# Optimization experiments

Hardware: AMD Instinct MI355X
Metric: run time of the kernel (lower is better)

Reference implementation:

```python
import jax, jax.numpy as jnp
import numpy as np

ALPHA = 0.2  # LeakyReLU negative slope
NEG_INF = jnp.float32(-9e15)


def setup_inputs() -> dict:
    key = jax.random.key(0)
    k1, k2, k3, k4, k5, k6 = jax.random.split(key, 6)
    B, N, F_in, F_out = 8, 2048, 256, 64
    h = jax.random.normal(k1, (B, N, F_in), dtype=jnp.float32)
    adj = jax.random.randint(k2, (B, N, N), 0, 2, dtype=jnp.int32)
    level = jax.random.uniform(k3, (B, N), dtype=jnp.float32)
    node_type = jax.random.uniform(k4, (B, N, N), dtype=jnp.float32)
    W = jax.random.normal(k5, (F_in, F_out), dtype=jnp.float32) * 1.414 / np.sqrt(F_in)
    a = jax.random.normal(k6, (2 * F_out, 1), dtype=jnp.float32) * 1.414 / np.sqrt(2 * F_out)
    return {"h": h, "adj": adj, "level": level, "node_type": node_type, "W": W, "a": a}


def reference(h, adj, level, node_type, W, a):
    # h: [B,N,Fin], adj/node_type: [B,N,N], level: [B,N], W: [Fin,Fout], a: [2*Fout,1]
    F_out = W.shape[1]
    Wh = jnp.einsum('bnf,fo->bno', h, W)  # [B,N,Fout]
    # Additive attention decomposed: e[b,i,j] = a1.Wh_i + a2.Wh_j (no O(N^2*2F) tensor)
    a1 = a[:F_out, 0]
    a2 = a[F_out:, 0]
    f1 = Wh @ a1  # [B,N]
    f2 = Wh @ a2  # [B,N]
    e = jax.nn.leaky_relu(f1[:, :, None] + f2[:, None, :], negative_slope=ALPHA)  # [B,N,N]
    # gat_our=True path: node_type scales scores, level scales Wh
    e = e * node_type
    Wh = Wh * level[:, :, None]
    attention = jnp.where(adj > 0, e, NEG_INF)
    attention = jax.nn.softmax(attention, axis=1)  # faithful: original softmax over dim=1
    # dropout p=0 / eval mode -> identity
    h_prime = jnp.einsum('bij,bjo->bio', attention, Wh)  # [B,N,Fout]
    return jax.nn.relu(h_prime)  # concat=True
```

## Files before the change

### kernel.cpp

```cpp
#include <hip/hip_runtime.h>

#define BB 8
#define NN 2048
#define FIN 256
#define FO 64

typedef short short8_t __attribute__((ext_vector_type(8)));
typedef float float4_t __attribute__((ext_vector_type(4)));
typedef int int4_v __attribute__((ext_vector_type(4)));

__device__ __forceinline__ unsigned short f2bf(float x) {
  unsigned int u = __float_as_uint(x);
  unsigned int r = (u + 0x7fffu + ((u >> 16) & 1u)) >> 16;
  return (unsigned short)r;
}

#define GLD16(gp, lp)                                                          \
  __builtin_amdgcn_global_load_lds(                                            \
      (const __attribute__((address_space(1))) void*)(gp),                     \
      (__attribute__((address_space(3))) void*)(lp), 16, 0, 0)

__global__ __launch_bounds__(256) void k1_fused(
    const float* __restrict__ h,
    const float* __restrict__ level,
    const float* __restrict__ W,
    const float* __restrict__ a,
    float* __restrict__ V, float* __restrict__ f1, float* __restrict__ f2,
    float* __restrict__ scol,
    const int* __restrict__ adj,
    unsigned int* __restrict__ abits)
{
  __shared__ float wlds[128 * 64];
  __shared__ float hs[16 * 260];
  __shared__ float parts1[16 * 17];
  __shared__ float parts2[16 * 17];
  int t = threadIdx.x;

  if (blockIdx.x >= 1024) {
    size_t g = (size_t)(blockIdx.x - 1024) * 256 + t;
    const int4_v* ap = (const int4_v*)adj + g * 8;
    int4_v av[8];
    #pragma unroll
    for (int e = 0; e < 8; ++e) av[e] = ap[e];
    unsigned int m = 0;
    #pragma unroll
    for (int e = 0; e < 8; ++e) {
      m |= (av[e].x > 0 ? 1u : 0u) << (4 * e);
      m |= (av[e].y > 0 ? 1u : 0u) << (4 * e + 1);
      m |= (av[e].z > 0 ? 1u : 0u) << (4 * e + 2);
      m |= (av[e].w > 0 ? 1u : 0u) << (4 * e + 3);
    }
    abits[g] = m;
    return;
  }

  int b = blockIdx.x >> 7;
  int i0 = (blockIdx.x & 127) * 16;

  if (blockIdx.x < 64) scol[blockIdx.x * 256 + t] = 0.0f;

  {
    int r_ld = t >> 4, f0 = (t & 15) * 16;
    const float* hp = h + (size_t)(b * NN + i0 + r_ld) * FIN + f0;
    float4 x0 = *(const float4*)(hp);
    float4 x1 = *(const float4*)(hp + 4);
    float4 x2 = *(const float4*)(hp + 8);
    float4 x3 = *(const float4*)(hp + 12);
    float* hd = &hs[r_ld * 260 + f0];
    *(float4*)(hd + 0) = x0; *(float4*)(hd + 4) = x1;
    *(float4*)(hd + 8) = x2; *(float4*)(hd + 12) = x3;
  }

  int r = t >> 4;
  int c4 = (t & 15) * 4;
  float4 acc = {0, 0, 0, 0};

  #pragma unroll
  for (int half = 0; half < 2; ++half) {
    __syncthreads();
    #pragma unroll
    for (int q = 0; q < 8; ++q) {
      int idx = q * 1024 + t * 4;
      *(float4*)&wlds[idx] = *(const float4*)&W[half * 8192 + idx];
    }
    __syncthreads();
    for (int f = 0; f < 128; f += 8) {
      float4 hv0 = *(const float4*)&hs[r * 260 + half * 128 + f];
      float4 hv1 = *(const float4*)&hs[r * 260 + half * 128 + f + 4];
      float hvv[8] = {hv0.x, hv0.y, hv0.z, hv0.w, hv1.x, hv1.y, hv1.z, hv1.w};
      #pragma unroll
      for (int k = 0; k < 8; ++k) {
        float4 wv = *(const float4*)&wlds[(f + k) * 64 + c4];
        acc.x += hvv[k] * wv.x; acc.y += hvv[k] * wv.y;
        acc.z += hvv[k] * wv.z; acc.w += hvv[k] * wv.w;
      }
    }
  }

  float p1 = acc.x * a[c4] + acc.y * a[c4 + 1] + acc.z * a[c4 + 2] + acc.w * a[c4 + 3];
  float p2 = acc.x * a[64 + c4] + acc.y * a[64 + c4 + 1] +
             acc.z * a[64 + c4 + 2] + acc.w * a[64 + c4 + 3];
  parts1[r * 17 + (t & 15)] = p1;
  parts2[r * 17 + (t & 15)] = p2;
  __syncthreads();
  if (t < 16) {
    float s1 = 0.f, s2 = 0.f;
    #pragma unroll
    for (int g = 0; g < 16; ++g) { s1 += parts1[t * 17 + g]; s2 += parts2[t * 17 + g]; }
    f1[b * NN + i0 + t] = s1;
    f2[b * NN + i0 + t] = s2;
  }

  float lv = level[b * NN + i0 + r];
  float4 vv = {acc.x * lv, acc.y * lv, acc.z * lv, acc.w * lv};
  *(float4*)&V[(size_t)(b * NN + i0 + r) * FO + c4] = vv;
}

__global__ __launch_bounds__(512) void k2a_stream(
    const unsigned int* __restrict__ abits,
    const float* __restrict__ ntp,
    const float* __restrict__ f1,
    const float* __restrict__ f2,
    unsigned short* __restrict__ u_bf,
    float* __restrict__ partials)
{
  __shared__ unsigned int lbits[32 * 64];
  __shared__ float sf1[32];
  int t = threadIdx.x;
  int b = blockIdx.x >> 6;
  int rowblk = blockIdx.x & 63;
  int row0 = rowblk * 32;
  size_t base = (size_t)b * NN;
  int j0 = t * 4;

  {
    const uint4* src = (const uint4*)(abits + (base + row0) * 64);
    ((uint4*)lbits)[t] = src[t];
    if (t < 32) sf1[t] = f1[base + row0 + t];
  }

  float4 f2v = *(const float4*)(f2 + base + j0);
  float acc0 = 0.f, acc1 = 0.f, acc2 = 0.f, acc3 = 0.f;

  size_t rb = (base + row0) * (size_t)NN + j0;
  const float* np = ntp + rb;
  unsigned short* up = u_bf + rb;
  int wrd = t >> 3;
  int sh = (t & 7) * 4;

  __syncthreads();

  #pragma unroll
  for (int g = 0; g < 4; ++g) {
    float4 nv[8];
    #pragma unroll
    for (int rr = 0; rr < 8; ++rr)
      nv[rr] = *(const float4*)(np + (size_t)(g * 8 + rr) * NN);
    #pragma unroll
    for (int rr = 0; rr < 8; ++rr) {
      int r = g * 8 + rr;
      unsigned int nib = lbits[r * 64 + wrd] >> sh;
      float f1v = sf1[r];
      float x0 = f1v + f2v.x; x0 = fmaxf(x0, 0.2f * x0);
      float x1 = f1v + f2v.y; x1 = fmaxf(x1, 0.2f * x1);
      float x2 = f1v + f2v.z; x2 = fmaxf(x2, 0.2f * x2);
      float x3 = f1v + f2v.w; x3 = fmaxf(x3, 0.2f * x3);
      float u0 = (nib & 1u) ? __expf(x0 * nv[rr].x) : 0.0f;
      float u1 = (nib & 2u) ? __expf(x1 * nv[rr].y) : 0.0f;
      float u2 = (nib & 4u) ? __expf(x2 * nv[rr].z) : 0.0f;
      float u3 = (nib & 8u) ? __expf(x3 * nv[rr].w) : 0.0f;
      acc0 += u0; acc1 += u1; acc2 += u2; acc3 += u3;
      unsigned int p0 = (unsigned int)f2bf(u0) | ((unsigned int)f2bf(u1) << 16);
      unsigned int p1 = (unsigned int)f2bf(u2) | ((unsigned int)f2bf(u3) << 16);
      *(uint2*)(up + (size_t)r * NN) = make_uint2(p0, p1);
    }
  }

  *(float4*)(partials + (size_t)(b * 64 + rowblk) * NN + j0) =
      make_float4(acc0, acc1, acc2, acc3);
}

__global__ __launch_bounds__(512) void k2a_stream_adj(
    const int* __restrict__ adj,
    const float* __restrict__ ntp,
    const float* __restrict__ f1,
    const float* __restrict__ f2,
    unsigned short* __restrict__ u_bf,
    float* __restrict__ partials)
{
  int t = threadIdx.x;
  int b = blockIdx.x >> 6;
  int rowblk = blockIdx.x & 63;
  int row0 = rowblk * 32;
  size_t base = (size_t)b * NN;
  int j0 = t * 4;

  float4 f2v = *(const float4*)(f2 + base + j0);
  float acc0 = 0.f, acc1 = 0.f, acc2 = 0.f, acc3 = 0.f;

  size_t rb = (base + row0) * (size_t)NN + j0;
  const int* ap = adj + rb;
  const float* np = ntp + rb;
  unsigned short* up = u_bf + rb;
  const float* f1p = f1 + base + row0;

  #pragma unroll
  for (int g = 0; g < 4; ++g) {
    int4 av[8];
    float4 nv[8];
    #pragma unroll
    for (int rr = 0; rr < 8; ++rr) {
      av[rr] = *(const int4*)(ap + (size_t)(g * 8 + rr) * NN);
      nv[rr] = *(const float4*)(np + (size_t)(g * 8 + rr) * NN);
    }
    #pragma unroll
    for (int rr = 0; rr < 8; ++rr) {
      float f1v = f1p[g * 8 + rr];
      float x0 = f1v + f2v.x; x0 = fmaxf(x0, 0.2f * x0);
      float x1 = f1v + f2v.y; x1 = fmaxf(x1, 0.2f * x1);
      float x2 = f1v + f2v.z; x2 = fmaxf(x2, 0.2f * x2);
      float x3 = f1v + f2v.w; x3 = fmaxf(x3, 0.2f * x3);
      float u0 = (av[rr].x > 0) ? __expf(x0 * nv[rr].x) : 0.0f;
      float u1 = (av[rr].y > 0) ? __expf(x1 * nv[rr].y) : 0.0f;
      float u2 = (av[rr].z > 0) ? __expf(x2 * nv[rr].z) : 0.0f;
      float u3 = (av[rr].w > 0) ? __expf(x3 * nv[rr].w) : 0.0f;
      acc0 += u0; acc1 += u1; acc2 += u2; acc3 += u3;
      unsigned int p0 = (unsigned int)f2bf(u0) | ((unsigned int)f2bf(u1) << 16);
      unsigned int p1 = (unsigned int)f2bf(u2) | ((unsigned int)f2bf(u3) << 16);
      *(uint2*)(up + (size_t)(g * 8 + rr) * NN) = make_uint2(p0, p1);
    }
  }

  *(float4*)(partials + (size_t)(b * 64 + rowblk) * NN + j0) =
      make_float4(acc0, acc1, acc2, acc3);
}

template <int STORE_U>
__global__ __launch_bounds__(512) void k2a_stats(
    const int* __restrict__ adj,
    const float* __restrict__ ntp,
    const float* __restrict__ f1,
    const float* __restrict__ f2,
    unsigned short* __restrict__ u_bf,
    unsigned char* __restrict__ bits,
    float* __restrict__ scol)
{
  __shared__ int ladj[2][16 * 256];
  __shared__ float lnt[2][16 * 256];
  __shared__ float red[2048];
  int t = threadIdx.x;
  int b = blockIdx.x >> 6;
  int row0 = (blockIdx.x & 63) * 32;
  int w = t >> 6, l = t & 63;
  size_t base = (size_t)b * NN;

  auto stage = [&](int buf, int s) {
    int tile = s >> 3, c = s & 7;
    int r0 = row0 + tile * 16 + 2 * w;
    const int* ga = adj + (base + r0) * NN + c * 256 + l * 4;
    const float* gn = ntp + (base + r0) * NN + c * 256 + l * 4;
    GLD16(ga, &ladj[buf][(2 * w) * 256]);
    GLD16(ga + NN, &ladj[buf][(2 * w + 1) * 256]);
    GLD16(gn, &lnt[buf][(2 * w) * 256]);
    GLD16(gn + NN, &lnt[buf][(2 * w + 1) * 256]);
  };

  int jj = t & 255;
  int rh = t >> 8;

  float accJ[8];
  #pragma unroll
  for (int c = 0; c < 8; ++c) accJ[c] = 0.f;
  float f2v[8];
  #pragma unroll
  for (int c = 0; c < 8; ++c) f2v[c] = f2[base + c * 256 + jj];

  stage(0, 0);
  for (int s = 0; s < 16; ++s) {
    int buf = s & 1;
    __syncthreads();
    if (s < 15) stage(buf ^ 1, s + 1);
    int tile = s >> 3, c = s & 7;
    #pragma unroll
    for (int q = 0; q < 8; ++q) {
      int r = rh * 8 + q;
      int av = ladj[buf][r * 256 + jj];
      float nv = lnt[buf][r * 256 + jj];
      float f1v = f1[base + row0 + tile * 16 + r];
      float x = f1v + f2v[c];
      x = fmaxf(x, 0.2f * x);
      bool m = av > 0;
      float u = m ? __expf(x * nv) : 0.0f;
      accJ[c] += u;
      if (STORE_U) {
        u_bf[(base + row0 + tile * 16 + r) * NN + c * 256 + jj] = f2bf(u);
      } else {
        unsigned long long bal = __ballot(m);
        if (l == 0)
          *(unsigned long long*)&bits[(base + row0 + tile * 16 + r) * (NN / 8)
                                      + c * 32 + (w & 3) * 8] = bal;
      }
    }
  }

  if (rh == 0) {
    #pragma unroll
    for (int c = 0; c < 8; ++c) red[c * 256 + jj] = accJ[c];
  }
  __syncthreads();
  if (rh == 1) {
    #pragma unroll
    for (int c = 0; c < 8; ++c) red[c * 256 + jj] += accJ[c];
  }
  __syncthreads();
  #pragma unroll
  for (int q = 0; q < 4; ++q)
    atomicAdd(&scol[base + q * 512 + t], red[q * 512 + t]);
}

__global__ __launch_bounds__(256) void k2b_pack_p(
    const float* __restrict__ V,
    const float* __restrict__ partials,
    unsigned short* __restrict__ vf)
{
  __shared__ float sred[8 * 32];
  __shared__ float sinv[32];
  int t = threadIdx.x;
  int b = blockIdx.x >> 6;
  int kk = blockIdx.x & 63;

  {
    int tj = t & 31, tr = t >> 5;
    float s = 0.f;
    #pragma unroll
    for (int q = 0; q < 8; ++q)
      s += partials[(size_t)(b * 64 + tr * 8 + q) * NN + kk * 32 + tj];
    sred[tr * 32 + tj] = s;
  }
  __syncthreads();
  if (t < 32) {
    float tot = 0.f;
    #pragma unroll
    for (int g = 0; g < 8; ++g) tot += sred[g * 32 + t];
    sinv[t] = (tot > 0.f) ? (1.0f / tot) : 0.0f;
  }
  __syncthreads();

  int ng = t >> 6;
  int l = t & 63;
  int jb0 = (l >> 4) * 8;
  int jb = kk * 32 + jb0;
  int o = ng * 16 + (l & 15);
  unsigned int pk[4];
  #pragma unroll
  for (int p = 0; p < 4; ++p) {
    int jr0 = jb + 2 * p, jr1 = jb + 2 * p + 1;
    float i0 = sinv[jb0 + 2 * p];
    float i1 = sinv[jb0 + 2 * p + 1];
    float v0 = V[(size_t)(b * NN + jr0) * FO + o] * i0;
    float v1 = V[(size_t)(b * NN + jr1) * FO + o] * i1;
    pk[p] = (unsigned int)f2bf(v0) | ((unsigned int)f2bf(v1) << 16);
  }
  *(uint4*)(vf + (size_t)(((b * 64 + kk) * 4 + ng) * 64 + l) * 8) =
      make_uint4(pk[0], pk[1], pk[2], pk[3]);
}

__global__ __launch_bounds__(256) void k2b_pack(
    const float* __restrict__ V,
    const float* __restrict__ scol,
    unsigned short* __restrict__ vf)
{
  int t = threadIdx.x;
  int b = blockIdx.x >> 6;
  int kk = blockIdx.x & 63;
  int ng = t >> 6;
  int l = t & 63;
  int jb = kk * 32 + ((l >> 4) * 8);
  int o = ng * 16 + (l & 15);
  unsigned int pk[4];
  #pragma unroll
  for (int p = 0; p < 4; ++p) {
    int jr0 = jb + 2 * p, jr1 = jb + 2 * p + 1;
    float s0 = scol[b * NN + jr0];
    float s1 = scol[b * NN + jr1];
    float i0 = (s0 > 0.f) ? (1.0f / s0) : 0.0f;
    float i1 = (s1 > 0.f) ? (1.0f / s1) : 0.0f;
    float v0 = V[(size_t)(b * NN + jr0) * FO + o] * i0;
    float v1 = V[(size_t)(b * NN + jr1) * FO + o] * i1;
    pk[p] = (unsigned int)f2bf(v0) | ((unsigned int)f2bf(v1) << 16);
  }
  *(uint4*)(vf + (size_t)(((b * 64 + kk) * 4 + ng) * 64 + l) * 8) =
      make_uint4(pk[0], pk[1], pk[2], pk[3]);
}

__global__ __launch_bounds__(512, 4) void k3_agg_u3(
    const unsigned short* __restrict__ u_bf,
    const unsigned short* __restrict__ vf,
    float* __restrict__ outp)
{
  __shared__ float red[8 * 16 * 68];
  int t = threadIdx.x;
  int b = blockIdx.x >> 6;
  int tt = blockIdx.x & 63;
  int i0 = tt * 32;
  int w = t >> 6, l = t & 63;
  int col = l & 15, quad = l >> 4;
  const unsigned short* urow0 = u_bf + (size_t)(b * NN + i0 + col) * NN + quad * 8;
  const unsigned short* urow1 = urow0 + (size_t)16 * NN;
  const unsigned short* vbase = vf + (size_t)(b * 64) * 2048 + l * 8;

  float4_t acc[2][4];
  #pragma unroll
  for (int sgi = 0; sgi < 2; ++sgi)
    #pragma unroll
    for (int g = 0; g < 4; ++g) acc[sgi][g] = (float4_t){0, 0, 0, 0};

  int kk0 = w * 8;
  short8_t A0 = *(const short8_t*)(urow0 + kk0 * 32);
  short8_t A1 = *(const short8_t*)(urow1 + kk0 * 32);
  const unsigned short* vb0 = vbase + (size_t)kk0 * 2048;
  short8_t c0 = *(const short8_t*)(vb0);
  short8_t c1 = *(const short8_t*)(vb0 + 512);
  short8_t c2 = *(const short8_t*)(vb0 + 1024);
  short8_t c3 = *(const short8_t*)(vb0 + 1536);

  #pragma unroll
  for (int s = 0; s < 8; ++s) {
    short8_t nA0, nA1, n0, n1, n2, n3;
    if (s < 7) {
      int kk = w * 8 + s + 1;
      nA0 = *(const short8_t*)(urow0 + kk * 32);
      nA1 = *(const short8_t*)(urow1 + kk * 32);
      const unsigned short* vn = vbase + (size_t)kk * 2048;
      n0 = *(const short8_t*)(vn);
      n1 = *(const short8_t*)(vn + 512);
      n2 = *(const short8_t*)(vn + 1024);
      n3 = *(const short8_t*)(vn + 1536);
    }
    acc[0][0] = __builtin_amdgcn_mfma_f32_16x16x32_bf16(A0, c0, acc[0][0], 0, 0, 0);
    acc[0][1] = __builtin_amdgcn_mfma_f32_16x16x32_bf16(A0, c1, acc[0][1], 0, 0, 0);
    acc[0][2] = __builtin_amdgcn_mfma_f32_16x16x32_bf16(A0, c2, acc[0][2], 0, 0, 0);
    acc[0][3] = __builtin_amdgcn_mfma_f32_16x16x32_bf16(A0, c3, acc[0][3], 0, 0, 0);
    acc[1][0] = __builtin_amdgcn_mfma_f32_16x16x32_bf16(A1, c0, acc[1][0], 0, 0, 0);
    acc[1][1] = __builtin_amdgcn_mfma_f32_16x16x32_bf16(A1, c1, acc[1][1], 0, 0, 0);
    acc[1][2] = __builtin_amdgcn_mfma_f32_16x16x32_bf16(A1, c2, acc[1][2], 0, 0, 0);
    acc[1][3] = __builtin_amdgcn_mfma_f32_16x16x32_bf16(A1, c3, acc[1][3], 0, 0, 0);
    if (s < 7) { A0 = nA0; A1 = nA1; c0 = n0; c1 = n1; c2 = n2; c3 = n3; }
  }

  #pragma unroll
  for (int sub = 0; sub < 2; ++sub) {
    __syncthreads();
    #pragma unroll
    for (int r = 0; r < 4; ++r) {
      int rowi = quad * 4 + r;
      float* rp = &red[w * 1088 + rowi * 68 + col];
      rp[0] = acc[sub][0][r];
      rp[16] = acc[sub][1][r];
      rp[32] = acc[sub][2][r];
      rp[48] = acc[sub][3][r];
    }
    __syncthreads();
    if (t < 256) {
      int row = t >> 4, o4 = (t & 15) * 4;
      const float* rp = &red[row * 68 + o4];
      float4 s0 = *(const float4*)(rp);
      float4 s1 = *(const float4*)(rp + 1088);
      float4 s2 = *(const float4*)(rp + 2176);
      float4 s3 = *(const float4*)(rp + 3264);
      float4 s4 = *(const float4*)(rp + 4352);
      float4 s5 = *(const float4*)(rp + 5440);
      float4 s6 = *(const float4*)(rp + 6528);
      float4 s7 = *(const float4*)(rp + 7616);
      float4 o;
      o.x = fmaxf(s0.x + s1.x + s2.x + s3.x + s4.x + s5.x + s6.x + s7.x, 0.0f);
      o.y = fmaxf(s0.y + s1.y + s2.y + s3.y + s4.y + s5.y + s6.y + s7.y, 0.0f);
      o.z = fmaxf(s0.z + s1.z + s2.z + s3.z + s4.z + s5.z + s6.z + s7.z, 0.0f);
      o.w = fmaxf(s0.w + s1.w + s2.w + s3.w + s4.w + s5.w + s6.w + s7.w, 0.0f);
      *(float4*)&outp[(size_t)(b * NN + i0 + sub * 16 + row) * FO + o4] = o;
    }
  }
}

__global__ __launch_bounds__(256) void k3_agg_b(
    const float* __restrict__ ntp,
    const unsigned char* __restrict__ bits,
    const float* __restrict__ f1,
    const float* __restrict__ f2,
    const unsigned short* __restrict__ vf,
    float* __restrict__ outp)
{
  __shared__ float red[4 * 16 * 68];
  int t = threadIdx.x;
  int b = blockIdx.x >> 7;
  int i0 = (blockIdx.x & 127) * 16;
  int w = t >> 6, l = t & 63;
  int col = l & 15, quad = l >> 4;
  int gi = b * NN + i0 + col;
  float f1v = f1[gi];
  const float* ntrow = ntp + (size_t)gi * NN;
  const unsigned char* brow = bits + (size_t)gi * (NN / 8);
  float4_t acc0 = {0, 0, 0, 0}, acc1 = {0, 0, 0, 0}, acc2 = {0, 0, 0, 0}, acc3 = {0, 0, 0, 0};

  for (int s = 0; s < 16; ++s) {
    int kk = w * 16 + s;
    int jq = kk * 32 + quad * 8;
    unsigned int m8 = brow[jq >> 3];
    float4 n0 = *(const float4*)(ntrow + jq);
    float4 n1 = *(const float4*)(ntrow + jq + 4);
    float4 g0 = *(const float4*)(f2 + b * NN + jq);
    float4 g1 = *(const float4*)(f2 + b * NN + jq + 4);
    float f2v[8] = {g0.x, g0.y, g0.z, g0.w, g1.x, g1.y, g1.z, g1.w};
    float ntf[8] = {n0.x, n0.y, n0.z, n0.w, n1.x, n1.y, n1.z, n1.w};
    union { unsigned int u[4]; short8_t v; } A;
    #pragma unroll
    for (int p = 0; p < 4; ++p) {
      int e0 = 2 * p, e1 = 2 * p + 1;
      float x0 = f1v + f2v[e0]; x0 = fmaxf(x0, 0.2f * x0);
      float u0 = ((m8 >> e0) & 1u) ? __expf(x0 * ntf[e0]) : 0.0f;
      float x1 = f1v + f2v[e1]; x1 = fmaxf(x1, 0.2f * x1);
      float u1 = ((m8 >> e1) & 1u) ? __expf(x1 * ntf[e1]) : 0.0f;
      A.u[p] = (unsigned int)f2bf(u0) | ((unsigned int)f2bf(u1) << 16);
    }
    const unsigned short* vb = vf + (size_t)(b * 64 + kk) * 2048 + l * 8;
    short8_t bf0 = *(const short8_t*)(vb);
    short8_t bf1 = *(const short8_t*)(vb + 512);
    short8_t bf2 = *(const short8_t*)(vb + 1024);
    short8_t bf3 = *(const short8_t*)(vb + 1536);
    acc0 = __builtin_amdgcn_mfma_f32_16x16x32_bf16(A.v, bf0, acc0, 0, 0, 0);
    acc1 = __builtin_amdgcn_mfma_f32_16x16x32_bf16(A.v, bf1, acc1, 0, 0, 0);
    acc2 = __builtin_amdgcn_mfma_f32_16x16x32_bf16(A.v, bf2, acc2, 0, 0, 0);
    acc3 = __builtin_amdgcn_mfma_f32_16x16x32_bf16(A.v, bf3, acc3, 0, 0, 0);
  }

  #pragma unroll
  for (int r = 0; r < 4; ++r) {
    int rowi = quad * 4 + r;
    red[w * 1088 + rowi * 68 + 0 + col] = acc0[r];
    red[w * 1088 + rowi * 68 + 16 + col] = acc1[r];
    red[w * 1088 + rowi * 68 + 32 + col] = acc2[r];
    red[w * 1088 + rowi * 68 + 48 + col] = acc3[r];
  }
  __syncthreads();

  int row = t >> 4, o4 = (t & 15) * 4;
  const float* rp = &red[row * 68 + o4];
  float4 s0 = *(const float4*)(rp);
  float4 s1 = *(const float4*)(rp + 1088);
  float4 s2 = *(const float4*)(rp + 2176);
  float4 s3 = *(const float4*)(rp + 3264);
  float4 o;
  o.x = fmaxf(s0.x + s1.x + s2.x + s3.x, 0.0f);
  o.y = fmaxf(s0.y + s1.y + s2.y + s3.y, 0.0f);
  o.z = fmaxf(s0.z + s1.z + s2.z + s3.z, 0.0f);
  o.w = fmaxf(s0.w + s1.w + s2.w + s3.w, 0.0f);
  *(float4*)&outp[(size_t)(b * NN + i0 + row) * FO + o4] = o;
}

extern "C" void kernel_launch(void* const* d_in, const int* in_sizes, int n_in,
                              void* d_out, int out_size, void* d_ws, size_t ws_size,
                              hipStream_t stream) {
  const float* h = (const float*)d_in[0];
  const int* adj = (const int*)d_in[1];
  const float* level = (const float*)d_in[2];
  const float* ntm = (const float*)d_in[3];
  const float* W = (const float*)d_in[4];
  const float* a = (const float*)d_in[5];
  float* outp = (float*)d_out;

  float* V = (float*)d_ws;
  float* f1 = V + (size_t)BB * NN * FO;
  float* f2 = f1 + BB * NN;
  float* scol = f2 + BB * NN;
  unsigned short* vf = (unsigned short*)(scol + BB * NN);
  float* partials = (float*)(vf + (size_t)BB * NN * FO);
  unsigned int* abits = (unsigned int*)(partials + (size_t)BB * 64 * NN);
  char* tail = (char*)(abits + (size_t)BB * NN * (NN / 32));
  size_t fixed2 = (size_t)(tail - (char*)d_ws);
  size_t fixed1 = (size_t)((char*)abits - (char*)d_ws);
  size_t ubytes = (size_t)BB * NN * NN * 2;
  bool big2 = (ws_size >= fixed2 + ubytes);
  bool big1 = (ws_size >= fixed1 + ubytes);

  if (big2) {
    unsigned short* u_bf = (unsigned short*)tail;
    k1_fused<<<5120, 256, 0, stream>>>(h, level, W, a, V, f1, f2, scol, adj, abits);
    k2a_stream<<<512, 512, 0, stream>>>(abits, ntm, f1, f2, u_bf, partials);
    k2b_pack_p<<<512, 256, 0, stream>>>(V, partials, vf);
    k3_agg_u3<<<512, 512, 0, stream>>>(u_bf, vf, outp);
  } else if (big1) {
    unsigned short* u_bf = (unsigned short*)abits;
    k1_fused<<<1024, 256, 0, stream>>>(h, level, W, a, V, f1, f2, scol, adj, abits);
    k2a_stream_adj<<<512, 512, 0, stream>>>(adj, ntm, f1, f2, u_bf, partials);
    k2b_pack_p<<<512, 256, 0, stream>>>(V, partials, vf);
    k3_agg_u3<<<512, 512, 0, stream>>>(u_bf, vf, outp);
  } else {
    unsigned char* bits = (unsigned char*)abits;
    k1_fused<<<1024, 256, 0, stream>>>(h, level, W, a, V, f1, f2, scol, adj, abits);
    k2a_stats<0><<<512, 512, 0, stream>>>(adj, ntm, f1, f2, nullptr, bits, scol);
    k2b_pack<<<512, 256, 0, stream>>>(V, scol, vf);
    k3_agg_b<<<1024, 256, 0, stream>>>(ntm, bits, f1, f2, vf, outp);
  }
}
```

Before: 326.9 us.

## Interleave adj-pack and GEMM blocks in k1, halve k3 row tile to 16

In k1, the Wh GEMM blocks are now interleaved with the adjacency bit-packing blocks (every fifth block does the GEMM) rather than all sitting at the front of the grid. The W staging tile also shrinks to 64 rows, cutting shared memory so more blocks can fit per CU. The aggregation kernel now handles 16 rows per block with one A fragment, doubling the grid to 1024 blocks and dropping the second reduction pass. This aims to balance load and raise occupancy, at the cost of re-reading the V fragments twice as often across blocks.

```diff
diff --git a/kernel.cpp b/kernel.cpp
--- a/kernel.cpp
+++ b/kernel.cpp
@@ -30,34 +30,41 @@
     const int* __restrict__ adj,
     unsigned int* __restrict__ abits)
 {
-  __shared__ float wlds[128 * 64];
+  __shared__ float wlds[64 * 64];
   __shared__ float hs[16 * 260];
   __shared__ float parts1[16 * 17];
   __shared__ float parts2[16 * 17];
   int t = threadIdx.x;
 
-  if (blockIdx.x >= 1024) {
-    size_t g = (size_t)(blockIdx.x - 1024) * 256 + t;
-    const int4_v* ap = (const int4_v*)adj + g * 8;
-    int4_v av[8];
-    #pragma unroll
-    for (int e = 0; e < 8; ++e) av[e] = ap[e];
-    unsigned int m = 0;
-    #pragma unroll
-    for (int e = 0; e < 8; ++e) {
-      m |= (av[e].x > 0 ? 1u : 0u) << (4 * e);
-      m |= (av[e].y > 0 ? 1u : 0u) << (4 * e + 1);
-      m |= (av[e].z > 0 ? 1u : 0u) << (4 * e + 2);
-      m |= (av[e].w > 0 ? 1u : 0u) << (4 * e + 3);
-    }
-    abits[g] = m;
-    return;
-  }
-
-  int b = blockIdx.x >> 7;
-  int i0 = (blockIdx.x & 127) * 16;
-
-  if (blockIdx.x < 64) scol[blockIdx.x * 256 + t] = 0.0f;
+  int g;
+  if (gridDim.x > 1024) {
+    if ((blockIdx.x % 5) != 0) {
+      size_t sid = (size_t)(blockIdx.x - blockIdx.x / 5 - 1);
+      size_t gg = sid * 256 + t;
+      const int4_v* ap = (const int4_v*)adj + gg * 8;
+      int4_v av[8];
+      #pragma unroll
+      for (int e = 0; e < 8; ++e) av[e] = ap[e];
+      unsigned int m = 0;
+      #pragma unroll
+      for (int e = 0; e < 8; ++e) {
+        m |= (av[e].x > 0 ? 1u : 0u) << (4 * e);
+        m |= (av[e].y > 0 ? 1u : 0u) << (4 * e + 1);
+        m |= (av[e].z > 0 ? 1u : 0u) << (4 * e + 2);
+        m |= (av[e].w > 0 ? 1u : 0u) << (4 * e + 3);
+      }
+      abits[gg] = m;
+      return;
+    }
+    g = blockIdx.x / 5;
+  } else {
+    g = blockIdx.x;
+  }
+
+  int b = g >> 7;
+  int i0 = (g & 127) * 16;
+
+  if (g < 64) scol[g * 256 + t] = 0.0f;
 
   {
     int r_ld = t >> 4, f0 = (t & 15) * 16;
@@ -76,17 +83,17 @@
   float4 acc = {0, 0, 0, 0};
 
   #pragma unroll
-  for (int half = 0; half < 2; ++half) {
+  for (int qtr = 0; qtr < 4; ++qtr) {
     __syncthreads();
     #pragma unroll
-    for (int q = 0; q < 8; ++q) {
+    for (int q = 0; q < 4; ++q) {
       int idx = q * 1024 + t * 4;
-      *(float4*)&wlds[idx] = *(const float4*)&W[half * 8192 + idx];
+      *(float4*)&wlds[idx] = *(const float4*)&W[qtr * 4096 + idx];
     }
     __syncthreads();
-    for (int f = 0; f < 128; f += 8) {
-      float4 hv0 = *(const float4*)&hs[r * 260 + half * 128 + f];
-      float4 hv1 = *(const float4*)&hs[r * 260 + half * 128 + f + 4];
+    for (int f = 0; f < 64; f += 8) {
+      float4 hv0 = *(const float4*)&hs[r * 260 + qtr * 64 + f];
+      float4 hv1 = *(const float4*)&hs[r * 260 + qtr * 64 + f + 4];
       float hvv[8] = {hv0.x, hv0.y, hv0.z, hv0.w, hv1.x, hv1.y, hv1.z, hv1.w};
       #pragma unroll
       for (int k = 0; k < 8; ++k) {
@@ -106,7 +113,7 @@
   if (t < 16) {
     float s1 = 0.f, s2 = 0.f;
     #pragma unroll
-    for (int g = 0; g < 16; ++g) { s1 += parts1[t * 17 + g]; s2 += parts2[t * 17 + g]; }
+    for (int q = 0; q < 16; ++q) { s1 += parts1[t * 17 + q]; s2 += parts2[t * 17 + q]; }
     f1[b * NN + i0 + t] = s1;
     f2[b * NN + i0 + t] = s2;
   }
@@ -393,31 +400,27 @@
       make_uint4(pk[0], pk[1], pk[2], pk[3]);
 }
 
-__global__ __launch_bounds__(512, 4) void k3_agg_u3(
+__global__ __launch_bounds__(512, 4) void k3_agg_u4(
     const unsigned short* __restrict__ u_bf,
     const unsigned short* __restrict__ vf,
     float* __restrict__ outp)
 {
   __shared__ float red[8 * 16 * 68];
   int t = threadIdx.x;
-  int b = blockIdx.x >> 6;
-  int tt = blockIdx.x & 63;
-  int i0 = tt * 32;
+  int b = blockIdx.x >> 7;
+  int tt = blockIdx.x & 127;
+  int i0 = tt * 16;
   int w = t >> 6, l = t & 63;
   int col = l & 15, quad = l >> 4;
   const unsigned short* urow0 = u_bf + (size_t)(b * NN + i0 + col) * NN + quad * 8;
-  const unsigned short* urow1 = urow0 + (size_t)16 * NN;
   const unsigned short* vbase = vf + (size_t)(b * 64) * 2048 + l * 8;
 
-  float4_t acc[2][4];
-  #pragma unroll
-  for (int sgi = 0; sgi < 2; ++sgi)
-    #pragma unroll
-    for (int g = 0; g < 4; ++g) acc[sgi][g] = (float4_t){0, 0, 0, 0};
+  float4_t acc[4];
+  #pragma unroll
+  for (int g = 0; g < 4; ++g) acc[g] = (float4_t){0, 0, 0, 0};
 
   int kk0 = w * 8;
   short8_t A0 = *(const short8_t*)(urow0 + kk0 * 32);
-  short8_t A1 = *(const short8_t*)(urow1 + kk0 * 32);
   const unsigned short* vb0 = vbase + (size_t)kk0 * 2048;
   short8_t c0 = *(const short8_t*)(vb0);
   short8_t c1 = *(const short8_t*)(vb0 + 512);
@@ -426,59 +429,50 @@
 
   #pragma unroll
   for (int s = 0; s < 8; ++s) {
-    short8_t nA0, nA1, n0, n1, n2, n3;
+    short8_t nA0, n0, n1, n2, n3;
     if (s < 7) {
       int kk = w * 8 + s + 1;
       nA0 = *(const short8_t*)(urow0 + kk * 32);
-      nA1 = *(const short8_t*)(urow1 + kk * 32);
       const unsigned short* vn = vbase + (size_t)kk * 2048;
       n0 = *(const short8_t*)(vn);
       n1 = *(const short8_t*)(vn + 512);
       n2 = *(const short8_t*)(vn + 1024);
       n3 = *(const short8_t*)(vn + 1536);
     }
-    acc[0][0] = __builtin_amdgcn_mfma_f32_16x16x32_bf16(A0, c0, acc[0][0], 0, 0, 0);
-    acc[0][1] = __builtin_amdgcn_mfma_f32_16x16x32_bf16(A0, c1, acc[0][1], 0, 0, 0);
-    acc[0][2] = __builtin_amdgcn_mfma_f32_16x16x32_bf16(A0, c2, acc[0][2], 0, 0, 0);
-    acc[0][3] = __builtin_amdgcn_mfma_f32_16x16x32_bf16(A0, c3, acc[0][3], 0, 0, 0);
-    acc[1][0] = __builtin_amdgcn_mfma_f32_16x16x32_bf16(A1, c0, acc[1][0], 0, 0, 0);
-    acc[1][1] = __builtin_amdgcn_mfma_f32_16x16x32_bf16(A1, c1, acc[1][1], 0, 0, 0);
-    acc[1][2] = __builtin_amdgcn_mfma_f32_16x16x32_bf16(A1, c2, acc[1][2], 0, 0, 0);
-    acc[1][3] = __builtin_amdgcn_mfma_f32_16x16x32_bf16(A1, c3, acc[1][3], 0, 0, 0);
-    if (s < 7) { A0 = nA0; A1 = nA1; c0 = n0; c1 = n1; c2 = n2; c3 = n3; }
-  }
-
-  #pragma unroll
-  for (int sub = 0; sub < 2; ++sub) {
-    __syncthreads();
-    #pragma unroll
-    for (int r = 0; r < 4; ++r) {
-      int rowi = quad * 4 + r;
-      float* rp = &red[w * 1088 + rowi * 68 + col];
-      rp[0] = acc[sub][0][r];
-      rp[16] = acc[sub][1][r];
-      rp[32] = acc[sub][2][r];
-      rp[48] = acc[sub][3][r];
-    }
-    __syncthreads();
-    if (t < 256) {
-      int row = t >> 4, o4 = (t & 15) * 4;
-      const float* rp = &red[row * 68 + o4];
-      float4 s0 = *(const float4*)(rp);
-      float4 s1 = *(const float4*)(rp + 1088);
-      float4 s2 = *(const float4*)(rp + 2176);
-      float4 s3 = *(const float4*)(rp + 3264);
-      float4 s4 = *(const float4*)(rp + 4352);
-      float4 s5 = *(const float4*)(rp + 5440);
-      float4 s6 = *(const float4*)(rp + 6528);
-      float4 s7 = *(const float4*)(rp + 7616);
-      float4 o;
-      o.x = fmaxf(s0.x + s1.x + s2.x + s3.x + s4.x + s5.x + s6.x + s7.x, 0.0f);
-      o.y = fmaxf(s0.y + s1.y + s2.y + s3.y + s4.y + s5.y + s6.y + s7.y, 0.0f);
-      o.z = fmaxf(s0.z + s1.z + s2.z + s3.z + s4.z + s5.z + s6.z + s7.z, 0.0f);
-      o.w = fmaxf(s0.w + s1.w + s2.w + s3.w + s4.w + s5.w + s6.w + s7.w, 0.0f);
-      *(float4*)&outp[(size_t)(b * NN + i0 + sub * 16 + row) * FO + o4] = o;
-    }
+    acc[0] = __builtin_amdgcn_mfma_f32_16x16x32_bf16(A0, c0, acc[0], 0, 0, 0);
+    acc[1] = __builtin_amdgcn_mfma_f32_16x16x32_bf16(A0, c1, acc[1], 0, 0, 0);
+    acc[2] = __builtin_amdgcn_mfma_f32_16x16x32_bf16(A0, c2, acc[2], 0, 0, 0);
+    acc[3] = __builtin_amdgcn_mfma_f32_16x16x32_bf16(A0, c3, acc[3], 0, 0, 0);
+    if (s < 7) { A0 = nA0; c0 = n0; c1 = n1; c2 = n2; c3 = n3; }
+  }
+
+  #pragma unroll
+  for (int r = 0; r < 4; ++r) {
+    int rowi = quad * 4 + r;
+    float* rp = &red[w * 1088 + rowi * 68 + col];
+    rp[0] = acc[0][r];
+    rp[16] = acc[1][r];
+    rp[32] = acc[2][r];
+    rp[48] = acc[3][r];
+  }
+  __syncthreads();
+  if (t < 256) {
+    int row = t >> 4, o4 = (t & 15) * 4;
+    const float* rp = &red[row * 68 + o4];
+    float4 s0 = *(const float4*)(rp);
+    float4 s1 = *(const float4*)(rp + 1088);
+    float4 s2 = *(const float4*)(rp + 2176);
+    float4 s3 = *(const float4*)(rp + 3264);
+    float4 s4 = *(const float4*)(rp + 4352);
+    float4 s5 = *(const float4*)(rp + 5440);
+    float4 s6 = *(const float4*)(rp + 6528);
+    float4 s7 = *(const float4*)(rp + 7616);
+    float4 o;
+    o.x = fmaxf(s0.x + s1.x + s2.x + s3.x + s4.x + s5.x + s6.x + s7.x, 0.0f);
+    o.y = fmaxf(s0.y + s1.y + s2.y + s3.y + s4.y + s5.y + s6.y + s7.y, 0.0f);
+    o.z = fmaxf(s0.z + s1.z + s2.z + s3.z + s4.z + s5.z + s6.z + s7.z, 0.0f);
+    o.w = fmaxf(s0.w + s1.w + s2.w + s3.w + s4.w + s5.w + s6.w + s7.w, 0.0f);
+    *(float4*)&outp[(size_t)(b * NN + i0 + row) * FO + o4] = o;
   }
 }
 
@@ -587,13 +581,13 @@
     k1_fused<<<5120, 256, 0, stream>>>(h, level, W, a, V, f1, f2, scol, adj, abits);
     k2a_stream<<<512, 512, 0, stream>>>(abits, ntm, f1, f2, u_bf, partials);
     k2b_pack_p<<<512, 256, 0, stream>>>(V, partials, vf);
-    k3_agg_u3<<<512, 512, 0, stream>>>(u_bf, vf, outp);
+    k3_agg_u4<<<1024, 512, 0, stream>>>(u_bf, vf, outp);
   } else if (big1) {
     unsigned short* u_bf = (unsigned short*)abits;
     k1_fused<<<1024, 256, 0, stream>>>(h, level, W, a, V, f1, f2, scol, adj, abits);
     k2a_stream_adj<<<512, 512, 0, stream>>>(adj, ntm, f1, f2, u_bf, partials);
     k2b_pack_p<<<512, 256, 0, stream>>>(V, partials, vf);
-    k3_agg_u3<<<512, 512, 0, stream>>>(u_bf, vf, outp);
+    k3_agg_u4<<<1024, 512, 0, stream>>>(u_bf, vf, outp);
   } else {
     unsigned char* bits = (unsigned char*)abits;
     k1_fused<<<1024, 256, 0, stream>>>(h, level, W, a, V, f1, f2, scol, adj, abits);
```

New measurement: 327.2 us. No clear change (+0.1%).
